# Kernel optimization log

Measured on AMD Instinct MI355X. Metric: run time of the kernel, lower is better.

## Reference

```python
import math
import jax, jax.numpy as jnp
import numpy as np

NUM_HEADS = 16


def setup_inputs() -> dict:
    key = jax.random.key(0)
    ks = jax.random.split(key, 5)
    B, S, H = 2, 2048, 1024
    hidden_states = jax.random.normal(ks[0], (B, S, H), dtype=jnp.float32)
    # causal lower-triangular float mask [1, 1, S, S], as the module expects
    ltor_mask = jnp.tril(jnp.ones((S, S), dtype=jnp.float32))[None, None, :, :]
    # weights stored pre-transposed: y = x @ W + b (equivalent to torch Linear)
    W_qkv = jax.random.normal(ks[1], (H, 3 * H), dtype=jnp.float32) * (1.0 / math.sqrt(H))
    b_qkv = jnp.zeros((3 * H,), dtype=jnp.float32)
    W_dense = jax.random.normal(ks[2], (H, H), dtype=jnp.float32) * (1.0 / math.sqrt(H))
    b_dense = jnp.zeros((H,), dtype=jnp.float32)
    return {
        "hidden_states": hidden_states,
        "ltor_mask": ltor_mask,
        "W_qkv": W_qkv,
        "b_qkv": b_qkv,
        "W_dense": W_dense,
        "b_dense": b_dense,
    }


def reference(hidden_states, ltor_mask, W_qkv, b_qkv, W_dense, b_dense):
    B, S, H = hidden_states.shape
    nh = NUM_HEADS
    hd = H // nh

    # fused QKV projection: [B, S, 3H] -> split -> [B, nh, S, hd]
    qkv = hidden_states @ W_qkv + b_qkv
    q, k, v = jnp.split(qkv, 3, axis=-1)

    def to_heads(x):
        return x.reshape(B, S, nh, hd).transpose(0, 2, 1, 3)

    q, k, v = to_heads(q), to_heads(k), to_heads(v)

    # scaled dot-product scores [B, nh, S, S]
    scores = jnp.einsum("bhqd,bhkd->bhqk", q, k) / math.sqrt(hd)
    # mul/sub causal masking, exactly as the torch module does
    scores = scores * ltor_mask - 10000.0 * (1.0 - ltor_mask)
    probs = jax.nn.softmax(scores, axis=-1)
    # attention dropout omitted (eval mode / p=0.0)

    ctx = jnp.einsum("bhqk,bhkd->bhqd", probs, v)
    ctx = ctx.transpose(0, 2, 1, 3).reshape(B, S, H)

    out = ctx @ W_dense + b_dense
    # output dropout omitted (eval mode / p=0.0)
    return out
```

## Files before the change

### kernel.cpp

```cpp
#include <hip/hip_runtime.h>
#include <math.h>

#define BATCH 2
#define SEQ   2048
#define HID   1024
#define NHEAD 16
#define HDIM  64
#define MTOT  (BATCH * SEQ)
#define QKVN  (3 * HID)
#define HBUF  ((size_t)BATCH * NHEAD * SEQ * HDIM)

typedef _Float16 f16x8 __attribute__((ext_vector_type(8)));
typedef _Float16 f16x4 __attribute__((ext_vector_type(4)));
typedef float    f32x4 __attribute__((ext_vector_type(4)));

#define MFMA16(a, b, c) __builtin_amdgcn_mfma_f32_16x16x32_f16((a), (b), (c), 0, 0, 0)

#define GLDS16(gp, lp) __builtin_amdgcn_global_load_lds( \
    (const __attribute__((address_space(1))) void*)(gp), \
    (__attribute__((address_space(3))) void*)(lp), 16, 0, 0)

#if __has_builtin(__builtin_amdgcn_exp2f)
#define EXP2F(x) __builtin_amdgcn_exp2f(x)
#else
#define EXP2F(x) exp2f(x)
#endif

#define SCALE2 0.18033688011f
#define MASK2  -14426.950408f
#define BIAS2  -4.0f

__global__ __launch_bounds__(256) void prep_kernel(
    const float* __restrict__ hs, const float* __restrict__ Wqkv,
    const float* __restrict__ Wd, _Float16* __restrict__ A_h,
    _Float16* __restrict__ outQ, _Float16* __restrict__ outD)
{
    __shared__ _Float16 T[32][36];
    const int gid = blockIdx.x;
    const int tid = threadIdx.x;
    if (gid < 2048) {
        const int ci = gid * 256 + tid;
        const int m = ci >> 7, cc = ci & 127;
        const float* src = hs + (size_t)m * 1024 + cc * 8;
        f16x8 o;
#pragma unroll
        for (int j = 0; j < 8; ++j) o[j] = (_Float16)src[j];
        *(f16x8*)(A_h + (size_t)m * 1024 + ((cc >> 3) << 6)
                  + (((cc & 7) ^ (m & 7)) << 3)) = o;
        return;
    }
    const int tb = gid - 2048;
    const int bx = tb & 127, k0 = (tb >> 7) * 32;
    const float* in;
    _Float16* out;
    int N, n0;
    bool isQ;
    if (bx < 96) { in = Wqkv; out = outQ; N = QKVN; n0 = bx * 32; isQ = true; }
    else         { in = Wd;   out = outD; N = HID;  n0 = (bx - 96) * 32; isQ = false; }
    {
        const int r = tid >> 3, c4 = (tid & 7) * 4;
        float4 v = *(const float4*)(in + (size_t)(k0 + r) * N + n0 + c4);
        T[r][c4 + 0] = (_Float16)v.x;
        T[r][c4 + 1] = (_Float16)v.y;
        T[r][c4 + 2] = (_Float16)v.z;
        T[r][c4 + 3] = (_Float16)v.w;
    }
    __syncthreads();
    {
        const int nn = tid >> 3, k4 = (tid & 7) * 4;
        const int n = n0 + nn;
        f16x4 o;
        o[0] = T[k4 + 0][nn]; o[1] = T[k4 + 1][nn];
        o[2] = T[k4 + 2][nn]; o[3] = T[k4 + 3][nn];
        if (isQ) {
            const int cin = (((k0 >> 5) & 1) << 2) | (k4 >> 3);
            const int pos = cin ^ (n & 7);
            *(f16x4*)(out + (size_t)n * 1024 + (k0 & ~63) + pos * 8 + (k4 & 7)) = o;
        } else {
            const int pos = ((k4 >> 3) ^ (n & 3)), half = (k4 >> 2) & 1;
            *(f16x4*)(out + (size_t)n * 1024 + k0 + pos * 8 + half * 4) = o;
        }
    }
}

__global__ __launch_bounds__(512, 2) void qkv_gemm8(
    const _Float16* __restrict__ A, const _Float16* __restrict__ Bt,
    const float* __restrict__ bias, _Float16* __restrict__ base)
{
    __shared__ _Float16 S[2][2][16384];
    const int tid = threadIdx.x;
    const int w = tid >> 6, l = tid & 63;
    const int a = l & 15, q4 = l >> 4, a7 = a & 7;
    const int xc = blockIdx.x & 7, loc = blockIdx.x >> 3;
    const int bx = (xc & 1) * 6 + loc % 6;
    const int by = (xc >> 1) * 4 + loc / 6;
    const int m0 = by * 256, n0 = bx * 256;
    const int wm = (w >> 2) * 128, wn = (w & 3) * 64;

    const int srow = tid >> 3;
    const int scol = (tid & 7) * 8;
    const _Float16* gAs = A  + (size_t)(m0 + srow) * 1024 + scol;
    const _Float16* gBs = Bt + (size_t)(n0 + srow) * 1024 + scol;

    auto stage_u = [&](int u, int kt, int sl) {
        const size_t ko = (size_t)kt * 64;
        if (u < 4)
            GLDS16(gAs + (size_t)u * 65536 + ko, &S[sl][0][0] + u * 4096 + tid * 8);
        else
            GLDS16(gBs + (size_t)(u - 4) * 65536 + ko, &S[sl][1][0] + (u - 4) * 4096 + tid * 8);
    };

#pragma unroll
    for (int u = 0; u < 8; ++u) stage_u(u, 0, 0);
#pragma unroll
    for (int u = 0; u < 8; ++u) stage_u(u, 1, 1);
    asm volatile("s_waitcnt vmcnt(8)" ::: "memory");
    __builtin_amdgcn_sched_barrier(0);
    __builtin_amdgcn_s_barrier();

    f32x4 acc[8][4];
#pragma unroll
    for (int i = 0; i < 8; ++i)
#pragma unroll
        for (int j = 0; j < 4; ++j) acc[i][j] = (f32x4){0.f, 0.f, 0.f, 0.f};

#define FRG(SP, row_, ks_) \
    (*(const f16x8*)&(SP)[(row_) * 64 + ((((ks_) * 4 + q4) ^ a7) << 3)])

    for (int t = 0; t < 16; ++t) {
        const int sl = t & 1, nsl = sl ^ 1;
        const _Float16* sA = &S[sl][0][0];
        const _Float16* sB = &S[sl][1][0];
        const bool st = (t >= 1) & (t < 15);

        f16x8 afL[4][2], afH[4][2], bfL[2][2], bfH[2][2];

#pragma unroll
        for (int i = 0; i < 4; ++i) {
            afL[i][0] = FRG(sA, wm + i * 16 + a, 0);
            afL[i][1] = FRG(sA, wm + i * 16 + a, 1);
        }
#pragma unroll
        for (int j = 0; j < 2; ++j) {
            bfL[j][0] = FRG(sB, wn + j * 16 + a, 0);
            bfL[j][1] = FRG(sB, wn + j * 16 + a, 1);
        }
        if (st) { stage_u(0, t + 1, nsl); stage_u(1, t + 1, nsl); stage_u(2, t + 1, nsl); }
        __builtin_amdgcn_s_barrier();
        asm volatile("s_waitcnt lgkmcnt(0)" ::: "memory");
        __builtin_amdgcn_s_setprio(1);
#pragma unroll
        for (int i = 0; i < 4; ++i)
#pragma unroll
            for (int j = 0; j < 2; ++j) {
                acc[i][j] = MFMA16(afL[i][0], bfL[j][0], acc[i][j]);
                acc[i][j] = MFMA16(afL[i][1], bfL[j][1], acc[i][j]);
            }
        __builtin_amdgcn_s_setprio(0);
        __builtin_amdgcn_s_barrier();

#pragma unroll
        for (int j = 0; j < 2; ++j) {
            bfH[j][0] = FRG(sB, wn + 32 + j * 16 + a, 0);
            bfH[j][1] = FRG(sB, wn + 32 + j * 16 + a, 1);
        }
        if (st) { stage_u(3, t + 1, nsl); stage_u(4, t + 1, nsl); stage_u(5, t + 1, nsl); }
        __builtin_amdgcn_s_barrier();
        asm volatile("s_waitcnt lgkmcnt(0)" ::: "memory");
        __builtin_amdgcn_s_setprio(1);
#pragma unroll
        for (int i = 0; i < 4; ++i)
#pragma unroll
            for (int j = 0; j < 2; ++j) {
                acc[i][j + 2] = MFMA16(afL[i][0], bfH[j][0], acc[i][j + 2]);
                acc[i][j + 2] = MFMA16(afL[i][1], bfH[j][1], acc[i][j + 2]);
            }
        __builtin_amdgcn_s_setprio(0);
        __builtin_amdgcn_s_barrier();

#pragma unroll
        for (int i = 0; i < 4; ++i) {
            afH[i][0] = FRG(sA, wm + 64 + i * 16 + a, 0);
            afH[i][1] = FRG(sA, wm + 64 + i * 16 + a, 1);
        }
        if (st) { stage_u(6, t + 1, nsl); stage_u(7, t + 1, nsl); }
        __builtin_amdgcn_s_barrier();
        asm volatile("s_waitcnt lgkmcnt(0)" ::: "memory");
        __builtin_amdgcn_s_setprio(1);
#pragma unroll
        for (int i = 0; i < 4; ++i)
#pragma unroll
            for (int j = 0; j < 2; ++j) {
                acc[i + 4][j + 2] = MFMA16(afH[i][0], bfH[j][0], acc[i + 4][j + 2]);
                acc[i + 4][j + 2] = MFMA16(afH[i][1], bfH[j][1], acc[i + 4][j + 2]);
            }
        __builtin_amdgcn_s_setprio(0);
        __builtin_amdgcn_s_barrier();

        __builtin_amdgcn_s_setprio(1);
#pragma unroll
        for (int i = 0; i < 4; ++i)
#pragma unroll
            for (int j = 0; j < 2; ++j) {
                acc[i + 4][j] = MFMA16(afH[i][0], bfL[j][0], acc[i + 4][j]);
                acc[i + 4][j] = MFMA16(afH[i][1], bfL[j][1], acc[i + 4][j]);
            }
        __builtin_amdgcn_s_setprio(0);
        asm volatile("s_waitcnt vmcnt(0)" ::: "memory");
        __builtin_amdgcn_sched_barrier(0);
        __builtin_amdgcn_s_barrier();
    }
#undef FRG

#pragma unroll
    for (int j = 0; j < 4; ++j) {
        const int n = n0 + wn + 16 * j + a;
        const float bv = bias[n];
        const int tq = n >> 10, h = (n >> 6) & 15, d = n & 63;
#pragma unroll
        for (int i = 0; i < 8; ++i) {
            const int mb = m0 + wm + 16 * i + q4 * 4;
            const int bb = mb >> 11, sb = mb & 2047;
            if (tq == 2) {
                f16x4 ov;
#pragma unroll
                for (int r = 0; r < 4; ++r) ov[r] = (_Float16)(acc[i][j][r] + bv);
                const size_t off =
                    ((size_t)((bb * 16 + h) * 64 + d)) * 2048
                    + (sb & ~63)
                    + ((((sb >> 3) & 7) ^ (d & 7)) << 3) + (sb & 7);
                *(f16x4*)(base + 3 * HBUF + off) = ov;
            } else if (tq == 1) {
#pragma unroll
                for (int r = 0; r < 4; ++r) {
                    const int s = sb + r;
                    const _Float16 val = (_Float16)(acc[i][j][r] + bv);
                    const int dk = ((((d >> 3) ^ (s & 7)) & 7) << 3) | (d & 7);
                    base[HBUF + ((size_t)(bb * 16 + h) * 2048 + s) * 64 + dk] = val;
                }
            } else {
#pragma unroll
                for (int r = 0; r < 4; ++r) {
                    const _Float16 val = (_Float16)(acc[i][j][r] + bv);
                    base[((size_t)(bb * 16 + h) * 2048 + sb + r) * 64 + d] = val;
                }
            }
        }
    }
}

template<int EPI, int TM>
__global__ __launch_bounds__(256) void mfma_gemm(
    const _Float16* __restrict__ A, const _Float16* __restrict__ Bt,
    const float* __restrict__ bias, void* __restrict__ Cout,
    int M, int N, int K)
{
    __shared__ _Float16 As[TM * 32];
    __shared__ _Float16 Bs[128 * 32];
    constexpr int TI = TM / 32;
    constexpr int AR = TM / 4;

    const int tid = threadIdx.x;
    const int w = tid >> 6, l = tid & 63;
    const int a = l & 15, q4 = l >> 4;
    const int m0 = blockIdx.y * TM, n0 = blockIdx.x * 128;
    const int wm = (w >> 1) * (TM / 2), wn = (w & 1) * 64;

    f32x4 acc[TI][4];
#pragma unroll
    for (int i = 0; i < TI; ++i)
#pragma unroll
        for (int j = 0; j < 4; ++j) acc[i][j] = (f32x4){0.f, 0.f, 0.f, 0.f};

    const _Float16* gA = A + (size_t)(m0 + w * AR + (l >> 2)) * K + (l & 3) * 8;
    const _Float16* gB = Bt + (size_t)(n0 + w * 32 + (l >> 2)) * K + (l & 3) * 8;
    _Float16* sA = As + w * AR * 32;
    _Float16* sB = Bs + w * 1024;

    for (int k0 = 0; k0 < K; k0 += 32) {
#pragma unroll
        for (int u = 0; u < TM / 64; ++u)
            GLDS16(gA + (size_t)u * 16 * K + k0, sA + u * 512);
        GLDS16(gB + k0,          sB);
        GLDS16(gB + 16 * K + k0, sB + 512);
        __syncthreads();

        f16x8 af[TI], bf[4];
        const int pa = (q4 ^ (a & 3)) << 3;
#pragma unroll
        for (int i = 0; i < TI; ++i)
            af[i] = *(const f16x8*)&As[(wm + 16 * i + a) * 32 + pa];
#pragma unroll
        for (int j = 0; j < 4; ++j)
            bf[j] = *(const f16x8*)&Bs[(wn + 16 * j + a) * 32 + pa];
#pragma unroll
        for (int i = 0; i < TI; ++i)
#pragma unroll
            for (int j = 0; j < 4; ++j)
                acc[i][j] = MFMA16(af[i], bf[j], acc[i][j]);
        __syncthreads();
    }

    {
        float* C = (float*)Cout;
#pragma unroll
        for (int j = 0; j < 4; ++j) {
            const int n = n0 + wn + 16 * j + a;
            const float bv = bias[n];
#pragma unroll
            for (int i = 0; i < TI; ++i)
#pragma unroll
                for (int r = 0; r < 4; ++r) {
                    const int m = m0 + wm + 16 * i + q4 * 4 + r;
                    C[(size_t)m * N + n] = acc[i][j][r] + bv;
                }
        }
    }
}

__global__ __launch_bounds__(256, 2) void attn_mfma(
    const _Float16* __restrict__ qb, const _Float16* __restrict__ kb,
    const _Float16* __restrict__ vtb, _Float16* __restrict__ ctx)
{
    __shared__ _Float16 Ks[2][64 * 64];
    __shared__ _Float16 VT[2][64 * 64];
    __shared__ _Float16 Ps[4][16 * 64];

    const int bid = blockIdx.x;
    const int jj = bid >> 3;
    const int bhIdx = (bid & 7) * 4 + (jj >> 4);
    const int p = jj & 15;
    const int b = bhIdx >> 4, h = bhIdx & 15;
    const int tid = threadIdx.x;
    const int w = tid >> 6, l = tid & 63;
    const int a = l & 15, q4 = l >> 4, a7 = a & 7;
    const size_t bh  = ((size_t)b * NHEAD + h) * SEQ;
    const size_t bhd = ((size_t)b * NHEAD + h) * 64;

    const int qHi = (31 - p) * 64 + w * 16;
    const int qLo = p * 64 + w * 16;
    const int ntiles = 32 - p;

    f16x8 qfh[2], qfl[2];
    {
        const _Float16* qp = qb + (bh + qHi + a) * 64;
        qfh[0] = *(const f16x8*)(qp + q4 * 8);
        qfh[1] = *(const f16x8*)(qp + 32 + q4 * 8);
        const _Float16* ql = qb + (bh + qLo + a) * 64;
        qfl[0] = *(const f16x8*)(ql + q4 * 8);
        qfl[1] = *(const f16x8*)(ql + 32 + q4 * 8);
    }

    f32x4 Oh[4], Ol[4];
#pragma unroll
    for (int c = 0; c < 4; ++c) {
        Oh[c] = (f32x4){0.f, 0.f, 0.f, 0.f};
        Ol[c] = (f32x4){0.f, 0.f, 0.f, 0.f};
    }
    float lh = 0.f, ll = 0.f;

    const _Float16* kg = kb + (bh + w * 16) * 64 + l * 8;
    const int vrow = w * 16 + (l >> 3);
    const _Float16* vg = vtb + (bhd + vrow) * 2048 + (l & 7) * 8;
    _Float16* pbuf = &Ps[w][0];
    const int p0 = (q4 ^ a7) << 3;

    auto stage = [&](int t, int buf) {
        _Float16* ksl = &Ks[buf][0] + w * 1024 + l * 8;
        const _Float16* kt = kg + (size_t)t * 4096;
        GLDS16(kt,       ksl);
        GLDS16(kt + 512, ksl + 512);
        _Float16* vtl = &VT[buf][0] + vrow * 64 + (l & 7) * 8;
        GLDS16(vg + t * 64,            vtl);
        GLDS16(vg + t * 64 + 8 * 2048, vtl + 512);
    };

    stage(0, 0);

    for (int t = 0; t < ntiles; ++t) {
        __syncthreads();
        if (t + 1 < ntiles) stage(t + 1, (t + 1) & 1);

        const _Float16* ksb  = &Ks[t & 1][0];
        const _Float16* vbuf = &VT[t & 1][0];
        const int kt0 = t * 64;
        const bool doLo = (t <= p);

        f32x4 sh[4], sl[4];
#pragma unroll
        for (int n0 = 0; n0 < 4; ++n0) {
            f16x8 kf0 = *(const f16x8*)&ksb[(n0 * 16 + a) * 64 + p0];
            f16x8 kf1 = *(const f16x8*)&ksb[(n0 * 16 + a) * 64 + (p0 ^ 32)];
            f32x4 c = (f32x4){0.f, 0.f, 0.f, 0.f};
            c = MFMA16(kf0, qfh[0], c);
            c = MFMA16(kf1, qfh[1], c);
            sh[n0] = c;
            if (doLo) {
                f32x4 d = (f32x4){0.f, 0.f, 0.f, 0.f};
                d = MFMA16(kf0, qfl[0], d);
                d = MFMA16(kf1, qfl[1], d);
                sl[n0] = d;
            }
        }

        auto half_step = [&](f32x4 st[4], float& lrun, f32x4* O,
                             const bool maskT, const int qbase) {
            if (maskT) {
#pragma unroll
                for (int n0 = 0; n0 < 4; ++n0)
#pragma unroll
                    for (int r = 0; r < 4; ++r) {
                        const int kgl = kt0 + n0 * 16 + q4 * 4 + r;
                        st[n0][r] = (kgl > qbase + a) ? MASK2
                                                      : fmaf(st[n0][r], SCALE2, BIAS2);
                    }
            } else {
#pragma unroll
                for (int n0 = 0; n0 < 4; ++n0)
#pragma unroll
                    for (int r = 0; r < 4; ++r)
                        st[n0][r] = fmaf(st[n0][r], SCALE2, BIAS2);
            }
            float ls = 0.f;
#pragma unroll
            for (int n0 = 0; n0 < 4; ++n0)
#pragma unroll
                for (int r = 0; r < 4; ++r) {
                    const float pe = EXP2F(st[n0][r]);
                    st[n0][r] = pe;
                    ls += pe;
                }
            lrun += ls;
#pragma unroll
            for (int n0 = 0; n0 < 4; ++n0) {
                f16x4 pk;
#pragma unroll
                for (int r = 0; r < 4; ++r) pk[r] = (_Float16)st[n0][r];
                const int pos = (2 * n0 + (q4 >> 1)) ^ a7;
                *(f16x4*)&pbuf[a * 64 + pos * 8 + ((q4 & 1) << 2)] = pk;
            }
            f16x8 pf0 = *(const f16x8*)&pbuf[a * 64 + p0];
            f16x8 pf1 = *(const f16x8*)&pbuf[a * 64 + (p0 ^ 32)];
#pragma unroll
            for (int c = 0; c < 4; ++c) {
                f16x8 vf0 = *(const f16x8*)&vbuf[(c * 16 + a) * 64 + p0];
                f16x8 vf1 = *(const f16x8*)&vbuf[(c * 16 + a) * 64 + (p0 ^ 32)];
                O[c] = MFMA16(vf0, pf0, O[c]);
                O[c] = MFMA16(vf1, pf1, O[c]);
            }
        };

        half_step(sh, lh, Oh, t == 31 - p, qHi);
        if (doLo) half_step(sl, ll, Ol, t == p, qLo);
    }

    auto finish = [&](float lrun, const f32x4* O, const int qbase) {
        float lt = lrun;
        lt += __shfl_xor(lt, 16);
        lt += __shfl_xor(lt, 32);
        const float inv = 1.0f / lt;
        const size_t row = (size_t)b * SEQ + qbase + a;
#pragma unroll
        for (int c = 0; c < 4; ++c) {
            const int d0 = c * 16 + q4 * 4;
            const int kcol = h * 64 + (d0 & ~31)
                           + ((((d0 >> 3) & 3) ^ (a & 3)) << 3) + (d0 & 7);
            f16x4 ov;
#pragma unroll
            for (int r = 0; r < 4; ++r) ov[r] = (_Float16)(O[c][r] * inv);
            *(f16x4*)(ctx + row * HID + kcol) = ov;
        }
    };
    finish(lh, Oh, qHi);
    finish(ll, Ol, qLo);
}

extern "C" void kernel_launch(void* const* d_in, const int* in_sizes, int n_in,
                              void* d_out, int out_size, void* d_ws, size_t ws_size,
                              hipStream_t stream) {
    const float* hs   = (const float*)d_in[0];
    const float* Wqkv = (const float*)d_in[2];
    const float* bqkv = (const float*)d_in[3];
    const float* Wd   = (const float*)d_in[4];
    const float* bd   = (const float*)d_in[5];

    _Float16* A_h   = (_Float16*)d_ws;
    _Float16* WqkvT = A_h + (size_t)MTOT * HID;
    _Float16* WdT   = WqkvT + (size_t)QKVN * HID;
    _Float16* qbuf  = WdT + (size_t)HID * HID;
    _Float16* ctxb  = qbuf + 4 * HBUF;

    prep_kernel<<<6144, 256, 0, stream>>>(hs, Wqkv, Wd, A_h, WqkvT, WdT);

    qkv_gemm8<<<192, 512, 0, stream>>>(A_h, WqkvT, bqkv, qbuf);

    attn_mfma<<<512, 256, 0, stream>>>(
        qbuf, qbuf + HBUF, qbuf + 3 * HBUF, ctxb);

    mfma_gemm<1, 64><<<dim3(HID / 128, MTOT / 64), 256, 0, stream>>>(
        ctxb, WdT, bd, d_out, MTOT, HID, HID);
}
```

Baseline: 190.6 us.

## Prefetch next-tile LDS fragments and drop intra-iteration barriers in QKV GEMM

The QKV GEMM main loop no longer splits its global-to-LDS staging across three sub-phases, each fenced by barriers and lgkmcnt waits. It now issues all eight staging loads at the start of each iteration and keeps a single barrier at the end. The first A/B fragments for the next k-tile are read from LDS right after that barrier, so their latency overlaps the loop turnover instead of stalling the start of the next MFMA block. This cuts per-iteration synchronisation, but it raises register pressure because the fragments stay live across iterations, and it packs all global loads into one burst.

```diff
diff --git a/kernel.cpp b/kernel.cpp
--- a/kernel.cpp
+++ b/kernel.cpp
@@ -117,6 +117,7 @@
     asm volatile("s_waitcnt vmcnt(8)" ::: "memory");
     __builtin_amdgcn_sched_barrier(0);
     __builtin_amdgcn_s_barrier();
+    __builtin_amdgcn_sched_barrier(0);
 
     f32x4 acc[8][4];
 #pragma unroll
@@ -126,6 +127,22 @@
 
 #define FRG(SP, row_, ks_) \
     (*(const f16x8*)&(SP)[(row_) * 64 + ((((ks_) * 4 + q4) ^ a7) << 3)])
+
+    f16x8 afL[4][2], afH[4][2], bfL[2][2], bfH[2][2];
+    {
+        const _Float16* sA = &S[0][0][0];
+        const _Float16* sB = &S[0][1][0];
+#pragma unroll
+        for (int i = 0; i < 4; ++i) {
+            afL[i][0] = FRG(sA, wm + i * 16 + a, 0);
+            afL[i][1] = FRG(sA, wm + i * 16 + a, 1);
+        }
+#pragma unroll
+        for (int j = 0; j < 2; ++j) {
+            bfL[j][0] = FRG(sB, wn + j * 16 + a, 0);
+            bfL[j][1] = FRG(sB, wn + j * 16 + a, 1);
+        }
+    }
 
     for (int t = 0; t < 16; ++t) {
         const int sl = t & 1, nsl = sl ^ 1;
@@ -133,21 +150,11 @@
         const _Float16* sB = &S[sl][1][0];
         const bool st = (t >= 1) & (t < 15);
 
-        f16x8 afL[4][2], afH[4][2], bfL[2][2], bfH[2][2];
-
-#pragma unroll
-        for (int i = 0; i < 4; ++i) {
-            afL[i][0] = FRG(sA, wm + i * 16 + a, 0);
-            afL[i][1] = FRG(sA, wm + i * 16 + a, 1);
-        }
-#pragma unroll
-        for (int j = 0; j < 2; ++j) {
-            bfL[j][0] = FRG(sB, wn + j * 16 + a, 0);
-            bfL[j][1] = FRG(sB, wn + j * 16 + a, 1);
-        }
-        if (st) { stage_u(0, t + 1, nsl); stage_u(1, t + 1, nsl); stage_u(2, t + 1, nsl); }
-        __builtin_amdgcn_s_barrier();
-        asm volatile("s_waitcnt lgkmcnt(0)" ::: "memory");
+        if (st) {
+#pragma unroll
+            for (int u = 0; u < 8; ++u) stage_u(u, t + 1, nsl);
+        }
+
         __builtin_amdgcn_s_setprio(1);
 #pragma unroll
         for (int i = 0; i < 4; ++i)
@@ -157,16 +164,12 @@
                 acc[i][j] = MFMA16(afL[i][1], bfL[j][1], acc[i][j]);
             }
         __builtin_amdgcn_s_setprio(0);
-        __builtin_amdgcn_s_barrier();
 
 #pragma unroll
         for (int j = 0; j < 2; ++j) {
             bfH[j][0] = FRG(sB, wn + 32 + j * 16 + a, 0);
             bfH[j][1] = FRG(sB, wn + 32 + j * 16 + a, 1);
         }
-        if (st) { stage_u(3, t + 1, nsl); stage_u(4, t + 1, nsl); stage_u(5, t + 1, nsl); }
-        __builtin_amdgcn_s_barrier();
-        asm volatile("s_waitcnt lgkmcnt(0)" ::: "memory");
         __builtin_amdgcn_s_setprio(1);
 #pragma unroll
         for (int i = 0; i < 4; ++i)
@@ -176,16 +179,12 @@
                 acc[i][j + 2] = MFMA16(afL[i][1], bfH[j][1], acc[i][j + 2]);
             }
         __builtin_amdgcn_s_setprio(0);
-        __builtin_amdgcn_s_barrier();
 
 #pragma unroll
         for (int i = 0; i < 4; ++i) {
             afH[i][0] = FRG(sA, wm + 64 + i * 16 + a, 0);
             afH[i][1] = FRG(sA, wm + 64 + i * 16 + a, 1);
         }
-        if (st) { stage_u(6, t + 1, nsl); stage_u(7, t + 1, nsl); }
-        __builtin_amdgcn_s_barrier();
-        asm volatile("s_waitcnt lgkmcnt(0)" ::: "memory");
         __builtin_amdgcn_s_setprio(1);
 #pragma unroll
         for (int i = 0; i < 4; ++i)
@@ -194,10 +193,6 @@
                 acc[i + 4][j + 2] = MFMA16(afH[i][0], bfH[j][0], acc[i + 4][j + 2]);
                 acc[i + 4][j + 2] = MFMA16(afH[i][1], bfH[j][1], acc[i + 4][j + 2]);
             }
-        __builtin_amdgcn_s_setprio(0);
-        __builtin_amdgcn_s_barrier();
-
-        __builtin_amdgcn_s_setprio(1);
 #pragma unroll
         for (int i = 0; i < 4; ++i)
 #pragma unroll
@@ -206,9 +201,26 @@
                 acc[i + 4][j] = MFMA16(afH[i][1], bfL[j][1], acc[i + 4][j]);
             }
         __builtin_amdgcn_s_setprio(0);
+
         asm volatile("s_waitcnt vmcnt(0)" ::: "memory");
         __builtin_amdgcn_sched_barrier(0);
         __builtin_amdgcn_s_barrier();
+        __builtin_amdgcn_sched_barrier(0);
+
+        if (t < 15) {
+            const _Float16* nA = &S[nsl][0][0];
+            const _Float16* nB = &S[nsl][1][0];
+#pragma unroll
+            for (int i = 0; i < 4; ++i) {
+                afL[i][0] = FRG(nA, wm + i * 16 + a, 0);
+                afL[i][1] = FRG(nA, wm + i * 16 + a, 1);
+            }
+#pragma unroll
+            for (int j = 0; j < 2; ++j) {
+                bfL[j][0] = FRG(nB, wn + j * 16 + a, 0);
+                bfL[j][1] = FRG(nB, wn + j * 16 + a, 1);
+            }
+        }
     }
 #undef FRG
 
```

Result: faster. 186.0 us (-2.4%).

## Deepen QKV GEMM pipeline by staging two k-tiles ahead with quadrant-ordered LDS loads

Applied to the files above, without the earlier changes.

The QKV GEMM now prefetches tile t+2 into the slot currently being consumed. It issues each quadrant's global-to-LDS loads only after that quadrant's fragments have been read, and waits with partial vmcnt instead of draining to zero each iteration. The XOR swizzle moves from the prep kernel's stored layout into the global source address of the load, so A and W_qkv are written plainly. The LDS layout is reorganized by warp quadrant to match the staging order. The goal is to hide global load latency better, at the cost of more intricate barrier and waitcnt ordering that could race if misordered.

```diff
diff --git a/kernel.cpp b/kernel.cpp
--- a/kernel.cpp
+++ b/kernel.cpp
@@ -45,8 +45,7 @@
         f16x8 o;
 #pragma unroll
         for (int j = 0; j < 8; ++j) o[j] = (_Float16)src[j];
-        *(f16x8*)(A_h + (size_t)m * 1024 + ((cc >> 3) << 6)
-                  + (((cc & 7) ^ (m & 7)) << 3)) = o;
+        *(f16x8*)(A_h + (size_t)m * 1024 + cc * 8) = o;
         return;
     }
     const int tb = gid - 2048;
@@ -73,9 +72,7 @@
         o[0] = T[k4 + 0][nn]; o[1] = T[k4 + 1][nn];
         o[2] = T[k4 + 2][nn]; o[3] = T[k4 + 3][nn];
         if (isQ) {
-            const int cin = (((k0 >> 5) & 1) << 2) | (k4 >> 3);
-            const int pos = cin ^ (n & 7);
-            *(f16x4*)(out + (size_t)n * 1024 + (k0 & ~63) + pos * 8 + (k4 & 7)) = o;
+            *(f16x4*)(out + (size_t)n * 1024 + k0 + k4) = o;
         } else {
             const int pos = ((k4 >> 3) ^ (n & 3)), half = (k4 >> 2) & 1;
             *(f16x4*)(out + (size_t)n * 1024 + k0 + pos * 8 + half * 4) = o;
@@ -97,26 +94,29 @@
     const int m0 = by * 256, n0 = bx * 256;
     const int wm = (w >> 2) * 128, wn = (w & 3) * 64;
 
-    const int srow = tid >> 3;
-    const int scol = (tid & 7) * 8;
-    const _Float16* gAs = A  + (size_t)(m0 + srow) * 1024 + scol;
-    const _Float16* gBs = Bt + (size_t)(n0 + srow) * 1024 + scol;
-
-    auto stage_u = [&](int u, int kt, int sl) {
-        const size_t ko = (size_t)kt * 64;
-        if (u < 4)
-            GLDS16(gAs + (size_t)u * 65536 + ko, &S[sl][0][0] + u * 4096 + tid * 8);
-        else
-            GLDS16(gBs + (size_t)(u - 4) * 65536 + ko, &S[sl][1][0] + (u - 4) * 4096 + tid * 8);
+    const int csw = (((tid & 7) ^ ((tid >> 3) & 7)) << 3);
+    const _Float16* gA0 = A  + (size_t)(m0 + (tid >> 3)) * 1024 + csw;
+    const _Float16* gB0 = Bt + (size_t)(n0 + (tid >> 8) * 64 + ((tid >> 3) & 31)) * 1024 + csw;
+
+    auto stageA = [&](int q, int kt, int sl) {
+#pragma unroll
+        for (int u = 0; u < 2; ++u)
+            GLDS16(gA0 + (size_t)(u * 128 + q * 64) * 1024 + kt * 64,
+                   &S[sl][0][0] + q * 8192 + u * 4096 + tid * 8);
     };
-
-#pragma unroll
-    for (int u = 0; u < 8; ++u) stage_u(u, 0, 0);
-#pragma unroll
-    for (int u = 0; u < 8; ++u) stage_u(u, 1, 1);
+    auto stageB = [&](int q, int kt, int sl) {
+#pragma unroll
+        for (int u = 0; u < 2; ++u)
+            GLDS16(gB0 + (size_t)(u * 128 + q * 32) * 1024 + kt * 64,
+                   &S[sl][1][0] + q * 8192 + u * 4096 + tid * 8);
+    };
+
+    stageA(0, 0, 0); stageB(0, 0, 0); stageA(1, 0, 0); stageB(1, 0, 0);
+    stageA(0, 1, 1); stageB(0, 1, 1); stageA(1, 1, 1); stageB(1, 1, 1);
     asm volatile("s_waitcnt vmcnt(8)" ::: "memory");
     __builtin_amdgcn_sched_barrier(0);
     __builtin_amdgcn_s_barrier();
+    __builtin_amdgcn_sched_barrier(0);
 
     f32x4 acc[8][4];
 #pragma unroll
@@ -124,93 +124,102 @@
 #pragma unroll
         for (int j = 0; j < 4; ++j) acc[i][j] = (f32x4){0.f, 0.f, 0.f, 0.f};
 
-#define FRG(SP, row_, ks_) \
-    (*(const f16x8*)&(SP)[(row_) * 64 + ((((ks_) * 4 + q4) ^ a7) << 3)])
-
+#define FA(SP, i_, ks_) (*(const f16x8*)&(SP)[ \
+    ((((i_) >> 2) * 128 + (w >> 2) * 64 + ((i_) & 3) * 16 + a) * 64) \
+    + ((((ks_) * 4 + q4) ^ a7) << 3)])
+#define FB(SP, j_, ks_) (*(const f16x8*)&(SP)[ \
+    ((((j_) >> 1) * 128 + (w & 3) * 32 + ((j_) & 1) * 16 + a) * 64) \
+    + ((((ks_) * 4 + q4) ^ a7) << 3)])
+#define BAR()  __builtin_amdgcn_sched_barrier(0); __builtin_amdgcn_s_barrier(); \
+               __builtin_amdgcn_sched_barrier(0)
+#define LGKM0() asm volatile("s_waitcnt lgkmcnt(0)" ::: "memory"); \
+               __builtin_amdgcn_sched_barrier(0)
+
+#pragma unroll 2
     for (int t = 0; t < 16; ++t) {
-        const int sl = t & 1, nsl = sl ^ 1;
+        const int sl = t & 1;
         const _Float16* sA = &S[sl][0][0];
         const _Float16* sB = &S[sl][1][0];
-        const bool st = (t >= 1) & (t < 15);
-
-        f16x8 afL[4][2], afH[4][2], bfL[2][2], bfH[2][2];
+        const bool st = (t < 14);
+
+        f16x8 aL[4][2], aH[4][2], bL[2][2], bH[2][2];
 
 #pragma unroll
         for (int i = 0; i < 4; ++i) {
-            afL[i][0] = FRG(sA, wm + i * 16 + a, 0);
-            afL[i][1] = FRG(sA, wm + i * 16 + a, 1);
+            aL[i][0] = FA(sA, i, 0); aL[i][1] = FA(sA, i, 1);
         }
 #pragma unroll
         for (int j = 0; j < 2; ++j) {
-            bfL[j][0] = FRG(sB, wn + j * 16 + a, 0);
-            bfL[j][1] = FRG(sB, wn + j * 16 + a, 1);
-        }
-        if (st) { stage_u(0, t + 1, nsl); stage_u(1, t + 1, nsl); stage_u(2, t + 1, nsl); }
-        __builtin_amdgcn_s_barrier();
-        asm volatile("s_waitcnt lgkmcnt(0)" ::: "memory");
+            bL[j][0] = FB(sB, j, 0); bL[j][1] = FB(sB, j, 1);
+        }
+        asm volatile("s_waitcnt lgkmcnt(8)" ::: "memory");
+        BAR();
+        LGKM0();
         __builtin_amdgcn_s_setprio(1);
 #pragma unroll
         for (int i = 0; i < 4; ++i)
 #pragma unroll
             for (int j = 0; j < 2; ++j) {
-                acc[i][j] = MFMA16(afL[i][0], bfL[j][0], acc[i][j]);
-                acc[i][j] = MFMA16(afL[i][1], bfL[j][1], acc[i][j]);
+                acc[i][j] = MFMA16(aL[i][0], bL[j][0], acc[i][j]);
+                acc[i][j] = MFMA16(aL[i][1], bL[j][1], acc[i][j]);
             }
         __builtin_amdgcn_s_setprio(0);
-        __builtin_amdgcn_s_barrier();
+        BAR();
 
 #pragma unroll
         for (int j = 0; j < 2; ++j) {
-            bfH[j][0] = FRG(sB, wn + 32 + j * 16 + a, 0);
-            bfH[j][1] = FRG(sB, wn + 32 + j * 16 + a, 1);
-        }
-        if (st) { stage_u(3, t + 1, nsl); stage_u(4, t + 1, nsl); stage_u(5, t + 1, nsl); }
-        __builtin_amdgcn_s_barrier();
-        asm volatile("s_waitcnt lgkmcnt(0)" ::: "memory");
+            bH[j][0] = FB(sB, j + 2, 0); bH[j][1] = FB(sB, j + 2, 1);
+        }
+        if (st) { stageA(0, t + 2, sl); stageB(0, t + 2, sl); }
+        BAR();
+        LGKM0();
         __builtin_amdgcn_s_setprio(1);
 #pragma unroll
         for (int i = 0; i < 4; ++i)
 #pragma unroll
             for (int j = 0; j < 2; ++j) {
-                acc[i][j + 2] = MFMA16(afL[i][0], bfH[j][0], acc[i][j + 2]);
-                acc[i][j + 2] = MFMA16(afL[i][1], bfH[j][1], acc[i][j + 2]);
+                acc[i][j + 2] = MFMA16(aL[i][0], bH[j][0], acc[i][j + 2]);
+                acc[i][j + 2] = MFMA16(aL[i][1], bH[j][1], acc[i][j + 2]);
             }
         __builtin_amdgcn_s_setprio(0);
-        __builtin_amdgcn_s_barrier();
+        BAR();
 
 #pragma unroll
         for (int i = 0; i < 4; ++i) {
-            afH[i][0] = FRG(sA, wm + 64 + i * 16 + a, 0);
-            afH[i][1] = FRG(sA, wm + 64 + i * 16 + a, 1);
-        }
-        if (st) { stage_u(6, t + 1, nsl); stage_u(7, t + 1, nsl); }
-        __builtin_amdgcn_s_barrier();
-        asm volatile("s_waitcnt lgkmcnt(0)" ::: "memory");
+            aH[i][0] = FA(sA, i + 4, 0); aH[i][1] = FA(sA, i + 4, 1);
+        }
+        if (st) stageB(1, t + 2, sl);
+        BAR();
+        LGKM0();
         __builtin_amdgcn_s_setprio(1);
 #pragma unroll
         for (int i = 0; i < 4; ++i)
 #pragma unroll
             for (int j = 0; j < 2; ++j) {
-                acc[i + 4][j + 2] = MFMA16(afH[i][0], bfH[j][0], acc[i + 4][j + 2]);
-                acc[i + 4][j + 2] = MFMA16(afH[i][1], bfH[j][1], acc[i + 4][j + 2]);
+                acc[i + 4][j + 2] = MFMA16(aH[i][0], bH[j][0], acc[i + 4][j + 2]);
+                acc[i + 4][j + 2] = MFMA16(aH[i][1], bH[j][1], acc[i + 4][j + 2]);
             }
         __builtin_amdgcn_s_setprio(0);
-        __builtin_amdgcn_s_barrier();
-
+        BAR();
+
+        if (st) stageA(1, t + 2, sl);
         __builtin_amdgcn_s_setprio(1);
 #pragma unroll
         for (int i = 0; i < 4; ++i)
 #pragma unroll
             for (int j = 0; j < 2; ++j) {
-                acc[i + 4][j] = MFMA16(afH[i][0], bfL[j][0], acc[i + 4][j]);
-                acc[i + 4][j] = MFMA16(afH[i][1], bfL[j][1], acc[i + 4][j]);
+                acc[i + 4][j] = MFMA16(aH[i][0], bL[j][0], acc[i + 4][j]);
+                acc[i + 4][j] = MFMA16(aH[i][1], bL[j][1], acc[i + 4][j]);
             }
         __builtin_amdgcn_s_setprio(0);
-        asm volatile("s_waitcnt vmcnt(0)" ::: "memory");
-        __builtin_amdgcn_sched_barrier(0);
-        __builtin_amdgcn_s_barrier();
-    }
-#undef FRG
+        if (st)            asm volatile("s_waitcnt vmcnt(8)" ::: "memory");
+        else if (t == 14)  asm volatile("s_waitcnt vmcnt(0)" ::: "memory");
+        BAR();
+    }
+#undef FA
+#undef FB
+#undef BAR
+#undef LGKM0
 
 #pragma unroll
     for (int j = 0; j < 4; ++j) {
```

New measurement: 187.2 us. Within noise of the previous version (-1.8%).
